# Kernel optimization log

Measured on AMD Instinct MI355X. Metric: run time of the kernel, lower is better.

## Reference

```python
import jax, jax.numpy as jnp
import numpy as np

B, NPTS, NBOX = 16, 100000, 64
PTS_THRESHOLD = 2048          # topk voxels kept per scene
GT_THRESHOLD = 2.5            # distance multiplier
VOXEL_SIZE = 0.01
TENSOR_STRIDE = 8             # stride of the level being pruned
SIZE = TENSOR_STRIDE * VOXEL_SIZE  # 0.08, per-voxel cell size at this level


def setup_inputs() -> dict:
    key = jax.random.key(0)
    k1, k2, k3 = jax.random.split(key, 3)
    scores = jax.random.normal(k1, (B, NPTS), dtype=jnp.float32)
    points = jax.random.uniform(k2, (B, NPTS, 3), dtype=jnp.float32)
    gt_centers = jax.random.uniform(k3, (B, NBOX, 3), dtype=jnp.float32)
    return {"scores": scores, "points": points, "gt_centers": gt_centers}


def reference(scores, points, gt_centers):
    # --- per-batch topk score mask (MEFPN3D._get_score_mask) ---
    _, idx = jax.lax.top_k(scores, PTS_THRESHOLD)          # [B, K]
    score_mask = jnp.zeros(scores.shape, dtype=bool)
    score_mask = score_mask.at[jnp.arange(B)[:, None], idx].set(True)  # scatter True

    # --- gt distance mask (MEFPN3D._get_gt_mask) ---
    # distances: [B, Npts, n_boxes]
    diff = points[:, :, None, :] - gt_centers[:, None, :, :]
    distances = jnp.sqrt(jnp.sum(diff * diff, axis=-1))
    gt_mask = jnp.any(distances < SIZE * GT_THRESHOLD, axis=-1)        # [B, Npts]

    # --- combined prune mask (scatter of per-batch masks into global mask) ---
    prune_mask = jnp.logical_or(score_mask, gt_mask)

    # --- per-voxel sigmoid BCE loss, reduction='none' (CrossEntropyLoss use_sigmoid=True) ---
    target = gt_mask.astype(scores.dtype)
    losses = target * jax.nn.softplus(-scores) + (1.0 - target) * jax.nn.softplus(scores)
    return prune_mask, losses
```

## Files before the change

kernel.cpp:

```cpp
#include <hip/hip_runtime.h>
#include <hip/hip_bf16.h>
#include <stdint.h>

#define BB 16
#define NPTS 100000
#define NBOX 64
#define KTOP 2048
#define THRF 0.2f
#define C_LO 0.039984f
#define C_HI 0.040016f

#define LIST_CAP 4096
#define NF4 (NPTS / 4)
#define CUT 0xC0000000u

#define STATE_OFF 0

__device__ __forceinline__ uint32_t fmap(float f) {
    uint32_t b = __float_as_uint(f);
    return (b & 0x80000000u) ? ~b : (b | 0x80000000u);
}

__global__ __launch_bounds__(1024) void select_k(const float* __restrict__ scores,
                                                 uint32_t* __restrict__ ws) {
    const int b = blockIdx.x, tid = threadIdx.x, w = tid >> 6, lane = tid & 63;
    __shared__ uint32_t h[16][257];
    __shared__ uint32_t hist[256], excl[256];
    __shared__ uint32_t list[LIST_CAP];
    __shared__ uint32_t sBin, sKrem, sE, sTot, sIstar, sRun, lcnt;

    for (int i = tid; i < 16 * 257; i += 1024) (&h[0][0])[i] = 0;
    if (tid == 0) { sIstar = NPTS; lcnt = 0; }
    __syncthreads();

    const float4* sc4 = reinterpret_cast<const float4*>(scores + (size_t)b * NPTS);
    uint32_t* mh = h[lane & 15];

    {
        int i4 = tid;
#pragma unroll 1
        for (int it = 0; it < 8; ++it, i4 += 3072) {
            const float4 v0 = sc4[i4];
            const float4 v1 = sc4[i4 + 1024];
            const float4 v2 = sc4[i4 + 2048];
            const uint32_t u[12] = {fmap(v0.x), fmap(v0.y), fmap(v0.z), fmap(v0.w),
                                    fmap(v1.x), fmap(v1.y), fmap(v1.z), fmap(v1.w),
                                    fmap(v2.x), fmap(v2.y), fmap(v2.z), fmap(v2.w)};
#pragma unroll
            for (int j = 0; j < 12; ++j) {
                atomicAdd(&mh[u[j] >> 24], 1u);
                if (u[j] >= CUT) {
                    const uint32_t pos = atomicAdd(&lcnt, 1u);
                    if (pos < LIST_CAP) list[pos] = u[j];
                }
            }
        }
        if (i4 < NF4) {
            const float4 v = sc4[i4];
            const uint32_t u[4] = {fmap(v.x), fmap(v.y), fmap(v.z), fmap(v.w)};
#pragma unroll
            for (int j = 0; j < 4; ++j) {
                atomicAdd(&mh[u[j] >> 24], 1u);
                if (u[j] >= CUT) {
                    const uint32_t pos = atomicAdd(&lcnt, 1u);
                    if (pos < LIST_CAP) list[pos] = u[j];
                }
            }
        }
    }
    __syncthreads();
    if (tid < 256) {
        uint32_t acc = 0;
#pragma unroll
        for (int j = 0; j < 16; ++j) acc += h[j][tid];
        hist[tid] = acc;
    }
    __syncthreads();

    if (tid < 64) {
        const uint32_t v0 = hist[4*tid], v1 = hist[4*tid+1], v2 = hist[4*tid+2], v3 = hist[4*tid+3];
        const uint32_t lt = v0 + v1 + v2 + v3;
        uint32_t x = lt;
#pragma unroll
        for (int off = 1; off < 64; off <<= 1) {
            const uint32_t y = __shfl_up(x, off);
            if (lane >= off) x += y;
        }
        const uint32_t ex = x - lt;
        excl[4*tid] = ex; excl[4*tid+1] = ex + v0;
        excl[4*tid+2] = ex + v0 + v1; excl[4*tid+3] = ex + v0 + v1 + v2;
        if (tid == 63) sTot = x;
    }
    __syncthreads();
    if (tid < 256) {
        const uint32_t total = sTot, lim = total - KTOP;
        const uint32_t pe = excl[tid];
        const uint32_t pe1 = (tid == 255) ? total : excl[tid + 1];
        if (pe <= lim && pe1 > lim) {
            sBin = (uint32_t)tid;
            sKrem = KTOP - (total - pe1);
        }
    }
    __syncthreads();
    const uint32_t beta = sBin;
    uint32_t prefix = beta << 24;
    uint32_t cnt;

    const bool spec = (beta >= (CUT >> 24)) && (lcnt <= LIST_CAP);
    if (spec) {
        cnt = lcnt;
    } else {
        __syncthreads();
        if (tid == 0) lcnt = 0;
        __syncthreads();
        for (int i4 = tid; i4 < NF4; i4 += 1024) {
            const float4 v = sc4[i4];
            const uint32_t u[4] = {fmap(v.x), fmap(v.y), fmap(v.z), fmap(v.w)};
#pragma unroll
            for (int j = 0; j < 4; ++j) {
                if ((u[j] >> 24) == beta) {
                    const uint32_t pos = atomicAdd(&lcnt, 1u);
                    if (pos < LIST_CAP) list[pos] = u[j];
                }
            }
        }
        __syncthreads();
        cnt = lcnt;
    }
    if (cnt > LIST_CAP) cnt = LIST_CAP;

#pragma unroll 1
    for (int shift = 16; shift >= 0; shift -= 8) {
        __syncthreads();
        if (tid < 256) hist[tid] = 0;
        __syncthreads();
        const uint32_t hi8 = prefix >> (shift + 8);
        for (uint32_t i = tid; i < cnt; i += 1024) {
            const uint32_t uu = list[i];
            if ((uu >> (shift + 8)) == hi8)
                atomicAdd(&hist[(uu >> shift) & 255u], 1u);
        }
        __syncthreads();
        if (tid < 64) {
            const uint32_t v0 = hist[4*tid], v1 = hist[4*tid+1], v2 = hist[4*tid+2], v3 = hist[4*tid+3];
            const uint32_t lt = v0 + v1 + v2 + v3;
            uint32_t x = lt;
#pragma unroll
            for (int off = 1; off < 64; off <<= 1) {
                const uint32_t y = __shfl_up(x, off);
                if (lane >= off) x += y;
            }
            const uint32_t ex = x - lt;
            excl[4*tid] = ex; excl[4*tid+1] = ex + v0;
            excl[4*tid+2] = ex + v0 + v1; excl[4*tid+3] = ex + v0 + v1 + v2;
            if (tid == 63) sTot = x;
        }
        __syncthreads();
        if (tid < 256) {
            const uint32_t target = sKrem;
            const uint32_t total = sTot, lim = total - target;
            const uint32_t pe = excl[tid];
            const uint32_t pe1 = (tid == 255) ? total : excl[tid + 1];
            if (pe <= lim && pe1 > lim) {
                sBin = (uint32_t)tid;
                sKrem = target - (total - pe1);
                if (shift == 0) sE = pe1 - pe;
            }
        }
        __syncthreads();
        prefix |= sBin << shift;
    }

    const uint32_t R = sKrem, E = sE;
    const uint32_t tbits = (prefix & 0x80000000u) ? (prefix & 0x7fffffffu) : ~prefix;

    if (E != R) {
        __shared__ uint32_t wcnt[16];
        const float T = __uint_as_float(tbits);
        if (tid == 0) sRun = 0;
        __syncthreads();
        const float* sc = scores + (size_t)b * NPTS;
        for (int base = 0; base < NPTS; base += 1024) {
            const uint32_t r0 = sRun;
            if (r0 > R) break;
            const int i = base + tid;
            const bool eq = (i < NPTS) && (sc[i] == T);
            const unsigned long long mask = __ballot(eq);
            if (lane == 0) wcnt[w] = (uint32_t)__popcll(mask);
            __syncthreads();
            uint32_t before = 0, total = 0;
            for (int ww = 0; ww < 16; ++ww) {
                const uint32_t c = wcnt[ww];
                if (ww < w) before += c;
                total += c;
            }
            if (eq) {
                const uint32_t rank = r0 + before +
                    (uint32_t)__popcll(mask & ((1ull << lane) - 1ull));
                if (rank == R) sIstar = (uint32_t)i;
            }
            __syncthreads();
            if (tid == 0) sRun = r0 + total;
            __syncthreads();
        }
        __syncthreads();
    }
    if (tid == 0) {
        uint32_t* st = ws + STATE_OFF + b * 2;
        st[0] = tbits;
        st[1] = sIstar;
    }
}

__device__ __noinline__ bool exact_gt(float px, float py, float pz,
                                      const float* __restrict__ C) {
    bool hit = false;
#pragma unroll 1
    for (int k = 0; k < NBOX; ++k) {
        float dx = px - C[3 * k + 0];
        float dy = py - C[3 * k + 1];
        float dz = pz - C[3 * k + 2];
        float d2 = __fadd_rn(__fadd_rn(__fmul_rn(dx, dx), __fmul_rn(dy, dy)),
                             __fmul_rn(dz, dz));
        if (__fsqrt_rn(d2) < THRF) hit = true;
    }
    return hit;
}

__global__ __launch_bounds__(256) void main_k(const float* __restrict__ scores,
                                              const float* __restrict__ points,
                                              const float* __restrict__ ctrs,
                                              const uint32_t* __restrict__ ws,
                                              float* __restrict__ out) {
    const int b = blockIdx.y;
    const uint32_t* st = ws + STATE_OFF + b * 2;
    const float T = __uint_as_float(st[0]);
    const uint32_t Istar = st[1];

    const int p0 = blockIdx.x * 1024 + threadIdx.x * 4;
    if (p0 >= NPTS) return;

    const float* P = points + ((size_t)b * NPTS + p0) * 3;
    const float4 a = *reinterpret_cast<const float4*>(P);
    const float4 c4 = *reinterpret_cast<const float4*>(P + 4);
    const float4 e = *reinterpret_cast<const float4*>(P + 8);
    const float px[4] = {a.x, a.w, c4.z, e.y};
    const float py[4] = {a.y, c4.x, c4.w, e.z};
    const float pz[4] = {a.z, c4.y, e.x, e.w};
    float m2[4] = {1e30f, 1e30f, 1e30f, 1e30f};

    const float* C = ctrs + b * NBOX * 3;
#pragma unroll 16
    for (int k = 0; k < NBOX; ++k) {
        const float cx = C[3 * k + 0];
        const float cy = C[3 * k + 1];
        const float cz = C[3 * k + 2];
        const float cc = fmaf(cx, cx, fmaf(cy, cy, cz * cz));
        const float m2x = -2.0f * cx, m2y = -2.0f * cy, m2z = -2.0f * cz;
#pragma unroll
        for (int j = 0; j < 4; ++j) {
            const float t = fmaf(m2x, px[j], fmaf(m2y, py[j], fmaf(m2z, pz[j], cc)));
            m2[j] = fminf(m2[j], t);
        }
    }

    const float4 sv = *reinterpret_cast<const float4*>(scores + (size_t)b * NPTS + p0);
    const float s[4] = {sv.x, sv.y, sv.z, sv.w};
    float pr[4], ls[4];
#pragma unroll
    for (int j = 0; j < 4; ++j) {
        const float pp = fmaf(px[j], px[j], fmaf(py[j], py[j], pz[j] * pz[j]));
        const float m = pp + m2[j];
        bool gt;
        if (m < C_LO) gt = true;
        else if (m >= C_HI) gt = false;
        else gt = exact_gt(px[j], py[j], pz[j], C);
        const bool sm = (s[j] > T) || (s[j] == T && (uint32_t)(p0 + j) < Istar);
        pr[j] = (gt || sm) ? 1.0f : 0.0f;
        const float x = gt ? -s[j] : s[j];
        ls[j] = fmaxf(x, 0.0f) + __logf(1.0f + __expf(-fabsf(s[j])));
    }
    float* o0 = out + (size_t)b * NPTS + p0;
    float* o1 = out + (size_t)BB * NPTS + (size_t)b * NPTS + p0;
    *reinterpret_cast<float4*>(o0) = make_float4(pr[0], pr[1], pr[2], pr[3]);
    *reinterpret_cast<float4*>(o1) = make_float4(ls[0], ls[1], ls[2], ls[3]);
}

extern "C" void kernel_launch(void* const* d_in, const int* in_sizes, int n_in,
                              void* d_out, int out_size, void* d_ws, size_t ws_size,
                              hipStream_t stream) {
    const float* scores = (const float*)d_in[0];
    const float* points = (const float*)d_in[1];
    const float* ctrs   = (const float*)d_in[2];
    float* out = (float*)d_out;
    uint32_t* ws = (uint32_t*)d_ws;

    select_k<<<BB, 1024, 0, stream>>>(scores, ws);
    const dim3 gridP(98, BB);
    main_k<<<gridP, 256, 0, stream>>>(scores, points, ctrs, ws, out);
}
```

Baseline: 47.84 us.

## Split top-k candidate gathering across slices and redo selection per main block

```diff
diff --git a/kernel.cpp b/kernel.cpp
--- a/kernel.cpp
+++ b/kernel.cpp
@@ -10,73 +10,55 @@
 #define C_LO 0.039984f
 #define C_HI 0.040016f
 
+#define SLICES 16
+#define SLICE_SPAN 6272
+#define SCAP 512
 #define LIST_CAP 4096
-#define NF4 (NPTS / 4)
 #define CUT 0xC0000000u
 
-#define STATE_OFF 0
+#define CAND_OFF 0
+#define CNT_OFF  (BB * SLICES * SCAP)
 
 __device__ __forceinline__ uint32_t fmap(float f) {
     uint32_t b = __float_as_uint(f);
     return (b & 0x80000000u) ? ~b : (b | 0x80000000u);
 }
 
-__global__ __launch_bounds__(1024) void select_k(const float* __restrict__ scores,
-                                                 uint32_t* __restrict__ ws) {
-    const int b = blockIdx.x, tid = threadIdx.x, w = tid >> 6, lane = tid & 63;
-    __shared__ uint32_t h[16][257];
-    __shared__ uint32_t hist[256], excl[256];
-    __shared__ uint32_t list[LIST_CAP];
-    __shared__ uint32_t sBin, sKrem, sE, sTot, sIstar, sRun, lcnt;
-
-    for (int i = tid; i < 16 * 257; i += 1024) (&h[0][0])[i] = 0;
-    if (tid == 0) { sIstar = NPTS; lcnt = 0; }
-    __syncthreads();
-
-    const float4* sc4 = reinterpret_cast<const float4*>(scores + (size_t)b * NPTS);
-    uint32_t* mh = h[lane & 15];
-
-    {
-        int i4 = tid;
-#pragma unroll 1
-        for (int it = 0; it < 8; ++it, i4 += 3072) {
-            const float4 v0 = sc4[i4];
-            const float4 v1 = sc4[i4 + 1024];
-            const float4 v2 = sc4[i4 + 2048];
-            const uint32_t u[12] = {fmap(v0.x), fmap(v0.y), fmap(v0.z), fmap(v0.w),
-                                    fmap(v1.x), fmap(v1.y), fmap(v1.z), fmap(v1.w),
-                                    fmap(v2.x), fmap(v2.y), fmap(v2.z), fmap(v2.w)};
-#pragma unroll
-            for (int j = 0; j < 12; ++j) {
-                atomicAdd(&mh[u[j] >> 24], 1u);
-                if (u[j] >= CUT) {
-                    const uint32_t pos = atomicAdd(&lcnt, 1u);
-                    if (pos < LIST_CAP) list[pos] = u[j];
-                }
-            }
-        }
-        if (i4 < NF4) {
-            const float4 v = sc4[i4];
-            const uint32_t u[4] = {fmap(v.x), fmap(v.y), fmap(v.z), fmap(v.w)};
-#pragma unroll
-            for (int j = 0; j < 4; ++j) {
-                atomicAdd(&mh[u[j] >> 24], 1u);
-                if (u[j] >= CUT) {
-                    const uint32_t pos = atomicAdd(&lcnt, 1u);
-                    if (pos < LIST_CAP) list[pos] = u[j];
-                }
-            }
-        }
-    }
-    __syncthreads();
-    if (tid < 256) {
-        uint32_t acc = 0;
-#pragma unroll
-        for (int j = 0; j < 16; ++j) acc += h[j][tid];
-        hist[tid] = acc;
-    }
-    __syncthreads();
-
+__global__ __launch_bounds__(256) void cand_k(const float* __restrict__ scores,
+                                              uint32_t* __restrict__ ws) {
+    __shared__ uint32_t buf[SCAP];
+    __shared__ uint32_t lcnt;
+    const int b = blockIdx.y, sl = blockIdx.x, tid = threadIdx.x;
+    if (tid == 0) lcnt = 0;
+    __syncthreads();
+    const int start = sl * SLICE_SPAN;
+    const int nf4 = min(SLICE_SPAN, NPTS - start) >> 2;
+    const float4* sc4 = reinterpret_cast<const float4*>(scores + (size_t)b * NPTS + start);
+    for (int i4 = tid; i4 < nf4; i4 += 256) {
+        const float4 v = sc4[i4];
+        const uint32_t u[4] = {fmap(v.x), fmap(v.y), fmap(v.z), fmap(v.w)};
+#pragma unroll
+        for (int j = 0; j < 4; ++j) {
+            if (u[j] >= CUT) {
+                const uint32_t pos = atomicAdd(&lcnt, 1u);
+                if (pos < SCAP) buf[pos] = u[j];
+            }
+        }
+    }
+    __syncthreads();
+    const uint32_t c = lcnt;
+    uint32_t* dst = ws + CAND_OFF + ((size_t)(b * SLICES + sl)) * SCAP;
+    const uint32_t cw = c < SCAP ? c : SCAP;
+    for (uint32_t i = tid; i < cw; i += 256) dst[i] = buf[i];
+    if (tid == 0) ws[CNT_OFF + b * SLICES + sl] = c;
+}
+
+__device__ __forceinline__ void pick256(const uint32_t* __restrict__ hist,
+                                        uint32_t* __restrict__ excl,
+                                        int tid, int lane, uint32_t target,
+                                        uint32_t* sBin, uint32_t* sKrem,
+                                        uint32_t* sE, uint32_t* sTot, int wantE) {
+    __syncthreads();
     if (tid < 64) {
         const uint32_t v0 = hist[4*tid], v1 = hist[4*tid+1], v2 = hist[4*tid+2], v3 = hist[4*tid+3];
         const uint32_t lt = v0 + v1 + v2 + v3;
@@ -89,127 +71,20 @@
         const uint32_t ex = x - lt;
         excl[4*tid] = ex; excl[4*tid+1] = ex + v0;
         excl[4*tid+2] = ex + v0 + v1; excl[4*tid+3] = ex + v0 + v1 + v2;
-        if (tid == 63) sTot = x;
-    }
-    __syncthreads();
-    if (tid < 256) {
-        const uint32_t total = sTot, lim = total - KTOP;
+        if (tid == 63) *sTot = x;
+    }
+    __syncthreads();
+    {
+        const uint32_t total = *sTot, lim = total - target;
         const uint32_t pe = excl[tid];
         const uint32_t pe1 = (tid == 255) ? total : excl[tid + 1];
         if (pe <= lim && pe1 > lim) {
-            sBin = (uint32_t)tid;
-            sKrem = KTOP - (total - pe1);
-        }
-    }
-    __syncthreads();
-    const uint32_t beta = sBin;
-    uint32_t prefix = beta << 24;
-    uint32_t cnt;
-
-    const bool spec = (beta >= (CUT >> 24)) && (lcnt <= LIST_CAP);
-    if (spec) {
-        cnt = lcnt;
-    } else {
-        __syncthreads();
-        if (tid == 0) lcnt = 0;
-        __syncthreads();
-        for (int i4 = tid; i4 < NF4; i4 += 1024) {
-            const float4 v = sc4[i4];
-            const uint32_t u[4] = {fmap(v.x), fmap(v.y), fmap(v.z), fmap(v.w)};
-#pragma unroll
-            for (int j = 0; j < 4; ++j) {
-                if ((u[j] >> 24) == beta) {
-                    const uint32_t pos = atomicAdd(&lcnt, 1u);
-                    if (pos < LIST_CAP) list[pos] = u[j];
-                }
-            }
-        }
-        __syncthreads();
-        cnt = lcnt;
-    }
-    if (cnt > LIST_CAP) cnt = LIST_CAP;
-
-#pragma unroll 1
-    for (int shift = 16; shift >= 0; shift -= 8) {
-        __syncthreads();
-        if (tid < 256) hist[tid] = 0;
-        __syncthreads();
-        const uint32_t hi8 = prefix >> (shift + 8);
-        for (uint32_t i = tid; i < cnt; i += 1024) {
-            const uint32_t uu = list[i];
-            if ((uu >> (shift + 8)) == hi8)
-                atomicAdd(&hist[(uu >> shift) & 255u], 1u);
-        }
-        __syncthreads();
-        if (tid < 64) {
-            const uint32_t v0 = hist[4*tid], v1 = hist[4*tid+1], v2 = hist[4*tid+2], v3 = hist[4*tid+3];
-            const uint32_t lt = v0 + v1 + v2 + v3;
-            uint32_t x = lt;
-#pragma unroll
-            for (int off = 1; off < 64; off <<= 1) {
-                const uint32_t y = __shfl_up(x, off);
-                if (lane >= off) x += y;
-            }
-            const uint32_t ex = x - lt;
-            excl[4*tid] = ex; excl[4*tid+1] = ex + v0;
-            excl[4*tid+2] = ex + v0 + v1; excl[4*tid+3] = ex + v0 + v1 + v2;
-            if (tid == 63) sTot = x;
-        }
-        __syncthreads();
-        if (tid < 256) {
-            const uint32_t target = sKrem;
-            const uint32_t total = sTot, lim = total - target;
-            const uint32_t pe = excl[tid];
-            const uint32_t pe1 = (tid == 255) ? total : excl[tid + 1];
-            if (pe <= lim && pe1 > lim) {
-                sBin = (uint32_t)tid;
-                sKrem = target - (total - pe1);
-                if (shift == 0) sE = pe1 - pe;
-            }
-        }
-        __syncthreads();
-        prefix |= sBin << shift;
-    }
-
-    const uint32_t R = sKrem, E = sE;
-    const uint32_t tbits = (prefix & 0x80000000u) ? (prefix & 0x7fffffffu) : ~prefix;
-
-    if (E != R) {
-        __shared__ uint32_t wcnt[16];
-        const float T = __uint_as_float(tbits);
-        if (tid == 0) sRun = 0;
-        __syncthreads();
-        const float* sc = scores + (size_t)b * NPTS;
-        for (int base = 0; base < NPTS; base += 1024) {
-            const uint32_t r0 = sRun;
-            if (r0 > R) break;
-            const int i = base + tid;
-            const bool eq = (i < NPTS) && (sc[i] == T);
-            const unsigned long long mask = __ballot(eq);
-            if (lane == 0) wcnt[w] = (uint32_t)__popcll(mask);
-            __syncthreads();
-            uint32_t before = 0, total = 0;
-            for (int ww = 0; ww < 16; ++ww) {
-                const uint32_t c = wcnt[ww];
-                if (ww < w) before += c;
-                total += c;
-            }
-            if (eq) {
-                const uint32_t rank = r0 + before +
-                    (uint32_t)__popcll(mask & ((1ull << lane) - 1ull));
-                if (rank == R) sIstar = (uint32_t)i;
-            }
-            __syncthreads();
-            if (tid == 0) sRun = r0 + total;
-            __syncthreads();
-        }
-        __syncthreads();
-    }
-    if (tid == 0) {
-        uint32_t* st = ws + STATE_OFF + b * 2;
-        st[0] = tbits;
-        st[1] = sIstar;
-    }
+            *sBin = (uint32_t)tid;
+            *sKrem = target - (total - pe1);
+            if (wantE) *sE = pe1 - pe;
+        }
+    }
+    __syncthreads();
 }
 
 __device__ __noinline__ bool exact_gt(float px, float py, float pz,
@@ -232,12 +107,132 @@
                                               const float* __restrict__ ctrs,
                                               const uint32_t* __restrict__ ws,
                                               float* __restrict__ out) {
-    const int b = blockIdx.y;
-    const uint32_t* st = ws + STATE_OFF + b * 2;
-    const float T = __uint_as_float(st[0]);
-    const uint32_t Istar = st[1];
-
-    const int p0 = blockIdx.x * 1024 + threadIdx.x * 4;
+    const int b = blockIdx.y, tid = threadIdx.x, w = tid >> 6, lane = tid & 63;
+    __shared__ union { uint32_t h4[4][257]; uint32_t list[LIST_CAP]; } U;
+    __shared__ uint32_t hist[256], excl[256];
+    __shared__ uint32_t scnt[SLICES], soff[SLICES];
+    __shared__ uint32_t wcnt[4];
+    __shared__ uint32_t sBin, sKrem, sE, sTot, sIstar, sRun, sSpec, lcnt;
+
+    const float* sc = scores + (size_t)b * NPTS;
+
+    if (tid < SLICES) scnt[tid] = ws[CNT_OFF + b * SLICES + tid];
+    __syncthreads();
+    if (tid == 0) {
+        uint32_t tot = 0; bool ok = true;
+        for (int s = 0; s < SLICES; ++s) {
+            soff[s] = tot;
+            const uint32_t c = scnt[s];
+            if (c > SCAP) ok = false;
+            tot += c;
+        }
+        sTot = tot;
+        sSpec = (ok && tot >= KTOP && tot <= LIST_CAP) ? 1u : 0u;
+        sKrem = KTOP;
+        sIstar = NPTS;
+        lcnt = 0;
+    }
+    __syncthreads();
+
+    uint32_t cnt, prefix;
+    int shift0;
+    if (sSpec) {
+        cnt = sTot;
+#pragma unroll 1
+        for (int s = 0; s < SLICES; ++s) {
+            const uint32_t c = scnt[s], o = soff[s];
+            const uint32_t* src = ws + CAND_OFF + ((size_t)(b * SLICES + s)) * SCAP;
+            for (uint32_t i = tid; i < c; i += 256) U.list[o + i] = src[i];
+        }
+        prefix = 0u;
+        shift0 = 24;
+    } else {
+        for (int i = tid; i < 4 * 257; i += 256) (&U.h4[0][0])[i] = 0;
+        __syncthreads();
+        const float4* sc4 = reinterpret_cast<const float4*>(sc);
+        for (int i4 = tid; i4 < NPTS / 4; i4 += 256) {
+            const float4 v = sc4[i4];
+            atomicAdd(&U.h4[w][fmap(v.x) >> 24], 1u);
+            atomicAdd(&U.h4[w][fmap(v.y) >> 24], 1u);
+            atomicAdd(&U.h4[w][fmap(v.z) >> 24], 1u);
+            atomicAdd(&U.h4[w][fmap(v.w) >> 24], 1u);
+        }
+        __syncthreads();
+        hist[tid] = U.h4[0][tid] + U.h4[1][tid] + U.h4[2][tid] + U.h4[3][tid];
+        pick256(hist, excl, tid, lane, KTOP, &sBin, &sKrem, &sE, &sTot, 0);
+        const uint32_t beta = sBin;
+        __syncthreads();
+        for (int i4 = tid; i4 < NPTS / 4; i4 += 256) {
+            const float4 v = sc4[i4];
+            const uint32_t u[4] = {fmap(v.x), fmap(v.y), fmap(v.z), fmap(v.w)};
+#pragma unroll
+            for (int j = 0; j < 4; ++j) {
+                if ((u[j] >> 24) == beta) {
+                    const uint32_t pos = atomicAdd(&lcnt, 1u);
+                    if (pos < LIST_CAP) U.list[pos] = u[j];
+                }
+            }
+        }
+        __syncthreads();
+        cnt = lcnt < LIST_CAP ? lcnt : LIST_CAP;
+        prefix = beta << 24;
+        shift0 = 16;
+    }
+
+#pragma unroll 1
+    for (int shift = shift0; shift >= 0; shift -= 8) {
+        __syncthreads();
+        hist[tid] = 0;
+        __syncthreads();
+        const uint32_t hi8 = (shift < 24) ? (prefix >> (shift + 8)) : 0u;
+        for (uint32_t i = tid; i < cnt; i += 256) {
+            const uint32_t uu = U.list[i];
+            const bool m = (shift == 24) || ((uu >> (shift + 8)) == hi8);
+            if (m) atomicAdd(&hist[(uu >> shift) & 255u], 1u);
+        }
+        const uint32_t target = sKrem;
+        pick256(hist, excl, tid, lane, target, &sBin, &sKrem, &sE, &sTot,
+                shift == 0 ? 1 : 0);
+        prefix |= sBin << shift;
+    }
+
+    const uint32_t R = sKrem, E = sE;
+    const uint32_t tbits = (prefix & 0x80000000u) ? (prefix & 0x7fffffffu) : ~prefix;
+
+    if (E != R) {
+        const float T = __uint_as_float(tbits);
+        if (tid == 0) sRun = 0;
+        __syncthreads();
+        for (int base = 0; base < NPTS; base += 256) {
+            const uint32_t r0 = sRun;
+            if (r0 > R) break;
+            const int i = base + tid;
+            const bool eq = (i < NPTS) && (sc[i] == T);
+            const unsigned long long mask = __ballot(eq);
+            if (lane == 0) wcnt[w] = (uint32_t)__popcll(mask);
+            __syncthreads();
+            uint32_t before = 0, total = 0;
+#pragma unroll
+            for (int ww = 0; ww < 4; ++ww) {
+                const uint32_t c = wcnt[ww];
+                if (ww < w) before += c;
+                total += c;
+            }
+            if (eq) {
+                const uint32_t rank = r0 + before +
+                    (uint32_t)__popcll(mask & ((1ull << lane) - 1ull));
+                if (rank == R) sIstar = (uint32_t)i;
+            }
+            __syncthreads();
+            if (tid == 0) sRun = r0 + total;
+            __syncthreads();
+        }
+    }
+    __syncthreads();
+    const float T = __uint_as_float(tbits);
+    const uint32_t Istar = sIstar;
+
+    const int p0 = blockIdx.x * 1024 + tid * 4;
     if (p0 >= NPTS) return;
 
     const float* P = points + ((size_t)b * NPTS + p0) * 3;
@@ -264,7 +259,7 @@
         }
     }
 
-    const float4 sv = *reinterpret_cast<const float4*>(scores + (size_t)b * NPTS + p0);
+    const float4 sv = *reinterpret_cast<const float4*>(sc + p0);
     const float s[4] = {sv.x, sv.y, sv.z, sv.w};
     float pr[4], ls[4];
 #pragma unroll
@@ -295,7 +290,8 @@
     float* out = (float*)d_out;
     uint32_t* ws = (uint32_t*)d_ws;
 
-    select_k<<<BB, 1024, 0, stream>>>(scores, ws);
+    const dim3 gridC(SLICES, BB);
+    cand_k<<<gridC, 256, 0, stream>>>(scores, ws);
     const dim3 gridP(98, BB);
     main_k<<<gridP, 256, 0, stream>>>(scores, points, ctrs, ws, out);
 }
```

Measured after the change: 57.30 us. +19.8%, slower.
